# Kernel optimization log

Measured on AMD Instinct MI355X. Metric: run time of the kernel, lower is better.

Reference implementation:

```python
import jax, jax.numpy as jnp
import numpy as np

N_EMBD = 1024
HEAD_SIZE = 64

def setup_inputs() -> dict:
    key = jax.random.key(0)
    k1, k2, k3, k4 = jax.random.split(key, 4)
    x = jax.random.normal(k1, (8, 2048, N_EMBD), dtype=jnp.float32)
    s = 1.0 / np.sqrt(N_EMBD)
    Wk = jax.random.normal(k2, (HEAD_SIZE, N_EMBD), dtype=jnp.float32) * s
    Wq = jax.random.normal(k3, (HEAD_SIZE, N_EMBD), dtype=jnp.float32) * s
    Wv = jax.random.normal(k4, (HEAD_SIZE, N_EMBD), dtype=jnp.float32) * s
    return {"x": x, "Wk": Wk, "Wq": Wq, "Wv": Wv}

def reference(x, Wk, Wq, Wv):
    B, T, C = x.shape
    k = jnp.einsum('btc,hc->bth', x, Wk)  # [B,T,Hd]
    q = jnp.einsum('btc,hc->bth', x, Wq)
    v = jnp.einsum('btc,hc->bth', x, Wv)
    # NOTE: original scales by C**-0.5 where C = n_embd (not head_size)
    wei = jnp.einsum('bqh,bkh->bqk', q, k) * (C ** -0.5)  # [B,T,T]
    causal = jnp.tril(jnp.ones((T, T), dtype=bool))
    wei = jnp.where(causal, wei, -jnp.inf)
    wei = jax.nn.softmax(wei, axis=-1)
    out = jnp.einsum('bqk,bkh->bqh', wei, v)  # [B,T,Hd]
    return out
```

## Files before the change

kernel.cpp:

```cpp
#include <hip/hip_runtime.h>


typedef __attribute__((ext_vector_type(4))) short sv4;
typedef __attribute__((ext_vector_type(8))) short sv8;
typedef __attribute__((ext_vector_type(4))) float f32x4;

#define NB   8
#define TSEQ 2048
#define CDIM 1024
#define HD   64
#define MROWS (NB * TSEQ)

__device__ __forceinline__ short f2s(float f) {
  union { float f; unsigned u; } v; v.f = f;
  unsigned u = v.u;
  u += 0x7fffu + ((u >> 16) & 1u);
  return (short)(u >> 16);
}
__device__ __forceinline__ unsigned pk2(float lo, float hi) {
  return (unsigned)(unsigned short)f2s(lo) | ((unsigned)(unsigned short)f2s(hi) << 16);
}
__device__ __forceinline__ void glds16(const short* g, short* l) {
  __builtin_amdgcn_global_load_lds(
      (const __attribute__((address_space(1))) unsigned int*)g,
      (__attribute__((address_space(3))) unsigned int*)l, 16, 0, 0);
}

__global__ __launch_bounds__(256) void wcvt(
    const float* __restrict__ Wq, const float* __restrict__ Wk,
    const float* __restrict__ Wv, short* __restrict__ wb)
{
  int i = blockIdx.x * 256 + threadIdx.x;
  int t = i / 3072;
  int rem = i - t * 3072;
  int r = rem >> 4, s = rem & 15;
  int j = r >> 6, wrow = r & 63;
  const float* W = (j == 0) ? Wq : (j == 1) ? Wk : Wv;
  const float* src = W + (size_t)wrow * CDIM + t * 128 + ((s ^ (wrow & 7)) << 3);
  float4 a = *(const float4*)src;
  float4 b = *(const float4*)(src + 4);
  sv8 v = {f2s(a.x), f2s(a.y), f2s(a.z), f2s(a.w),
           f2s(b.x), f2s(b.y), f2s(b.z), f2s(b.w)};
  *(sv8*)(wb + (size_t)i * 8) = v;
}

__global__ __launch_bounds__(1024) void qkv_proj(
    const float* __restrict__ x,
    const short* __restrict__ wb,
    short* __restrict__ qw,
    short* __restrict__ kw,
    short* __restrict__ vtw)
{
  __shared__ short wlds[2][24576];
  __shared__ short xlds[2][8192];
  const int tid  = threadIdx.x;
  const int wid  = tid >> 6;
  const int lane = tid & 63;
  const int g    = lane >> 4;
  const int c16  = lane & 15;
  const int rowg = wid >> 2;
  const int ph   = wid & 3;
  const int row0 = blockIdx.x * 64;

  const int xr = tid >> 4, xs = tid & 15;
  const float* xsrc = x + (size_t)(row0 + xr) * CDIM + xs * 8;
  const int xwo = xr * 128 + ((xs ^ (xr & 7)) << 3);

  const int arow = rowg * 16 + c16;
  const int x7   = arow & 7;
  int rWo[3], rW7[3];
  #pragma unroll
  for (int p6 = 0; p6 < 3; ++p6) {
    int p = ph * 3 + p6;
    int r = (p >> 2) * 64 + (p & 3) * 16 + c16;
    rWo[p6] = r * 128;
    rW7[p6] = r & 7;
  }

  f32x4 acc[3];
  #pragma unroll
  for (int p6 = 0; p6 < 3; ++p6) acc[p6] = (f32x4){0.f, 0.f, 0.f, 0.f};

  float4 px[2][2];

  #pragma unroll
  for (int k2 = 0; k2 < 3; ++k2)
    glds16(wb + (size_t)(tid + k2 * 1024) * 8, &wlds[0][(tid + k2 * 1024) * 8]);
  px[0][0] = *(const float4*)(xsrc);
  px[0][1] = *(const float4*)(xsrc + 4);
  px[1][0] = *(const float4*)(xsrc + 128);
  px[1][1] = *(const float4*)(xsrc + 132);
  asm volatile("s_waitcnt vmcnt(2)" ::: "memory");
  {
    float4 A = px[0][0], B = px[0][1];
    sv8 v = {f2s(A.x), f2s(A.y), f2s(A.z), f2s(A.w),
             f2s(B.x), f2s(B.y), f2s(B.z), f2s(B.w)};
    *(sv8*)&xlds[0][xwo] = v;
  }
  asm volatile("s_waitcnt lgkmcnt(0)" ::: "memory");
  __builtin_amdgcn_sched_barrier(0);
  __builtin_amdgcn_s_barrier();

  #pragma unroll
  for (int t = 0; t < 8; ++t) {
    const int buf = t & 1;
    if (t < 7) {
      #pragma unroll
      for (int k2 = 0; k2 < 3; ++k2)
        glds16(wb + (size_t)((t + 1) * 3072 + tid + k2 * 1024) * 8,
               &wlds[buf ^ 1][(tid + k2 * 1024) * 8]);
    }
    if (t < 6) {
      px[t & 1][0] = *(const float4*)(xsrc + (t + 2) * 128);
      px[t & 1][1] = *(const float4*)(xsrc + (t + 2) * 128 + 4);
    }
    if (t < 7) {
      float4 A = px[(t + 1) & 1][0], B = px[(t + 1) & 1][1];
      sv8 v = {f2s(A.x), f2s(A.y), f2s(A.z), f2s(A.w),
               f2s(B.x), f2s(B.y), f2s(B.z), f2s(B.w)};
      *(sv8*)&xlds[buf ^ 1][xwo] = v;
    }
    #pragma unroll
    for (int kk = 0; kk < 4; ++kk) {
      int kslot = kk * 4 + g;
      sv8 a = *(const sv8*)&xlds[buf][arow * 128 + ((kslot ^ x7) << 3)];
      #pragma unroll
      for (int p6 = 0; p6 < 3; ++p6) {
        sv8 bfr = *(const sv8*)&wlds[buf][rWo[p6] + ((kslot ^ rW7[p6]) << 3)];
        acc[p6] = __builtin_amdgcn_mfma_f32_16x16x32_bf16(a, bfr, acc[p6], 0, 0, 0);
      }
    }
    if (t < 7) {
      if (t < 6) asm volatile("s_waitcnt vmcnt(2) lgkmcnt(0)" ::: "memory");
      else       asm volatile("s_waitcnt vmcnt(0) lgkmcnt(0)" ::: "memory");
      __builtin_amdgcn_sched_barrier(0);
      __builtin_amdgcn_s_barrier();
    }
  }

  #pragma unroll
  for (int p6 = 0; p6 < 3; ++p6) {
    int p = ph * 3 + p6, j = p >> 2, n = p & 3;
    int cc  = (n << 4) + c16;
    int rr0 = row0 + rowg * 16 + (g << 2);
    if (j == 2) {
      int b = rr0 >> 11, ti = rr0 & (TSEQ - 1);
      int kt = ti >> 6, key = ti & 63;
      sv4 v = {f2s(acc[p6][0]), f2s(acc[p6][1]), f2s(acc[p6][2]), f2s(acc[p6][3])};
      *(sv4*)&vtw[(((size_t)b * 32 + kt) * 64 + cc) * 64 +
                  ((((key >> 3) ^ (cc & 7)) << 3) | (key & 7))] = v;
    } else {
      #pragma unroll
      for (int r = 0; r < 4; ++r) {
        int rr = rr0 + r;
        if (j == 0) {
          qw[(size_t)rr * HD + cc] = f2s(acc[p6][r] * 0.03125f);
        } else {
          kw[(size_t)rr * HD + ((((cc >> 3) ^ (rr & 7)) << 3) | (cc & 7))] =
              f2s(acc[p6][r]);
        }
      }
    }
  }
}

__global__ __launch_bounds__(256) void attn(
    const short* __restrict__ qw,
    const short* __restrict__ kw,
    const short* __restrict__ vtw,
    float* __restrict__ Opart,
    float* __restrict__ mlws)
{
  __shared__ short kbuf[2][8192];
  __shared__ short vbuf[2][8192];
  __shared__ short bridge[4][2048];

  const int tid  = threadIdx.x;
  const int wid  = tid >> 6;
  const int lane = tid & 63;
  const int g    = lane >> 4;
  const int c16  = lane & 15;

  const int bid   = blockIdx.x;
  const int h     = bid >> 8;
  const int sub   = bid & 255;
  const int batch = sub & 7;
  const int jj    = sub >> 3;
  const int qb    = h ? (31 - jj) : jj;
  const int q0    = qb << 6;
  const size_t base = (size_t)batch * TSEQ * HD;

  const int ntot = (qb >> 1) + 1;
  const int th_  = (ntot + 1) >> 1;
  const int t0   = h ? th_ : 0;
  const int t1   = h ? ntot : th_;

  const int qrow = q0 + (wid << 4) + c16;
  sv8 qa0 = *(const sv8*)(qw + base + (size_t)qrow * HD + (g << 3));
  sv8 qa1 = *(const sv8*)(qw + base + (size_t)qrow * HD + 32 + (g << 3));

  float m = -1e30f, l = 0.f;
  f32x4 o[4];
  #pragma unroll
  for (int n = 0; n < 4; ++n) o[n] = (f32x4){0.f, 0.f, 0.f, 0.f};

  short* br = &bridge[wid][0];
  const int sx = c16 & 15;

  #define STAGE(tt, bb)                                                      \
    {                                                                        \
      const short* ksrc = kw + base + (size_t)(tt) * 8192;                   \
      const short* vsrc = vtw + ((size_t)batch * 32 + (tt) * 2) * 4096;      \
      _Pragma("unroll")                                                      \
      for (int q = 0; q < 4; ++q)                                            \
        glds16(ksrc + (tid + q * 256) * 8, &kbuf[bb][(tid + q * 256) * 8]);  \
      _Pragma("unroll")                                                      \
      for (int q = 0; q < 4; ++q)                                            \
        glds16(vsrc + (tid + q * 256) * 8, &vbuf[bb][(tid + q * 256) * 8]);  \
    }

  if (t0 < t1) {
    STAGE(t0, 0);
    asm volatile("s_waitcnt vmcnt(0)" ::: "memory");
    __builtin_amdgcn_s_barrier();

    for (int t = t0; t < t1; ++t) {
      const int buf = (t - t0) & 1;
      if (t + 1 < t1) STAGE(t + 1, buf ^ 1);

      f32x4 s[8];
      #pragma unroll
      for (int n = 0; n < 8; ++n) s[n] = (f32x4){0.f, 0.f, 0.f, 0.f};
      __builtin_amdgcn_s_setprio(1);
      #pragma unroll
      for (int n = 0; n < 8; ++n) {
        int kr = (n << 4) + c16;
        sv8 k0 = *(const sv8*)&kbuf[buf][kr * 64 + ((g ^ (kr & 7)) << 3)];
        s[n] = __builtin_amdgcn_mfma_f32_16x16x32_bf16(k0, qa0, s[n], 0, 0, 0);
        sv8 k1 = *(const sv8*)&kbuf[buf][kr * 64 + (((4 + g) ^ (kr & 7)) << 3)];
        s[n] = __builtin_amdgcn_mfma_f32_16x16x32_bf16(k1, qa1, s[n], 0, 0, 0);
      }
      __builtin_amdgcn_s_setprio(0);

      if (t == (qb >> 1)) {
        #pragma unroll
        for (int n = 0; n < 8; ++n) {
          int key = (t << 7) + (n << 4) + (g << 2);
          #pragma unroll
          for (int r = 0; r < 4; ++r)
            s[n][r] = (key + r <= qrow) ? s[n][r] : -1e30f;
        }
      }

      float pmax = -1e30f;
      #pragma unroll
      for (int n = 0; n < 8; ++n)
        pmax = fmaxf(pmax, fmaxf(fmaxf(s[n][0], s[n][1]), fmaxf(s[n][2], s[n][3])));
      float mnew  = m;
      float alpha = 1.f;
      const bool defer = (__all(pmax - m <= 8.0f) != 0);
      if (!defer) {
        float mx = fmaxf(pmax, __shfl_xor(pmax, 16));
        mx = fmaxf(mx, __shfl_xor(mx, 32));
        mnew  = fmaxf(m, mx);
        alpha = __expf(m - mnew);
        m = mnew;
      }

      float sum = 0.f;
      #pragma unroll
      for (int n = 0; n < 8; ++n) {
        float p0 = __expf(s[n][0] - mnew);
        float p1 = __expf(s[n][1] - mnew);
        float p2 = __expf(s[n][2] - mnew);
        float p3 = __expf(s[n][3] - mnew);
        sum += (p0 + p1) + (p2 + p3);
        int slot = 2 * n + (g >> 1);
        uint2 w2; w2.x = pk2(p0, p1); w2.y = pk2(p2, p3);
        *(uint2*)&br[c16 * 128 + ((slot ^ sx) << 3) + ((g & 1) << 2)] = w2;
      }
      sum += __shfl_xor(sum, 16);
      sum += __shfl_xor(sum, 32);

      if (!defer) {
        l = l * alpha + sum;
        float af[4];
        #pragma unroll
        for (int r = 0; r < 4; ++r) af[r] = __shfl(alpha, (g << 2) + r);
        #pragma unroll
        for (int n = 0; n < 4; ++n)
          #pragma unroll
          for (int r = 0; r < 4; ++r) o[n][r] *= af[r];
      } else {
        l += sum;
      }

      asm volatile("s_waitcnt lgkmcnt(0)" ::: "memory");
      __builtin_amdgcn_sched_barrier(0);

      __builtin_amdgcn_s_setprio(1);
      #pragma unroll
      for (int kk = 0; kk < 4; ++kk) {
        int kslot = (kk << 2) + g;
        sv8 pa = *(const sv8*)&br[c16 * 128 + ((kslot ^ sx) << 3)];
        #pragma unroll
        for (int n = 0; n < 4; ++n) {
          int vr = (n << 4) + c16;
          sv8 vf = *(const sv8*)&vbuf[buf][(kslot >> 3) * 4096 + vr * 64 +
                                           (((kslot & 7) ^ (vr & 7)) << 3)];
          o[n] = __builtin_amdgcn_mfma_f32_16x16x32_bf16(pa, vf, o[n], 0, 0, 0);
        }
      }
      __builtin_amdgcn_s_setprio(0);

      if (t + 1 < t1) {
        asm volatile("s_waitcnt vmcnt(0)" ::: "memory");
        __builtin_amdgcn_sched_barrier(0);
        __builtin_amdgcn_s_barrier();
      }
    }
  }

  #pragma unroll
  for (int n = 0; n < 4; ++n) {
    #pragma unroll
    for (int r = 0; r < 4; ++r) {
      int row = (wid << 4) + (g << 2) + r;
      Opart[(size_t)bid * 4096 + row * 64 + (n << 4) + c16] = o[n][r];
    }
  }
  if (lane < 16) {
    int row = (wid << 4) + lane;
    mlws[((size_t)bid * 64 + row) * 2]     = m;
    mlws[((size_t)bid * 64 + row) * 2 + 1] = l;
  }
  #undef STAGE
}

__global__ __launch_bounds__(256) void combine(
    const float* __restrict__ Opart,
    const float* __restrict__ mlws,
    float* __restrict__ out)
{
  const int bid   = blockIdx.x;
  const int batch = bid & 7;
  const int qb    = bid >> 3;
  const int q0    = qb << 6;
  const int bid0  = bid;
  const int bid1  = 256 + ((31 - qb) << 3) + batch;

  const int tid = threadIdx.x;
  const int row = tid >> 2;
  const int cs  = (tid & 3) << 4;

  float m0 = mlws[((size_t)bid0 * 64 + row) * 2];
  float l0 = mlws[((size_t)bid0 * 64 + row) * 2 + 1];
  float m1 = mlws[((size_t)bid1 * 64 + row) * 2];
  float l1 = mlws[((size_t)bid1 * 64 + row) * 2 + 1];
  float M  = fmaxf(m0, m1);
  float a0 = __expf(m0 - M), a1 = __expf(m1 - M);
  float invL = 1.f / (l0 * a0 + l1 * a1);

  const float* O0 = Opart + (size_t)bid0 * 4096 + row * 64 + cs;
  const float* O1 = Opart + (size_t)bid1 * 4096 + row * 64 + cs;
  float* op = out + ((size_t)batch * TSEQ + q0 + row) * HD + cs;

  #pragma unroll
  for (int e = 0; e < 4; ++e) {
    float4 v0 = *(const float4*)(O0 + e * 4);
    float4 v1 = *(const float4*)(O1 + e * 4);
    float4 res;
    res.x = (v0.x * a0 + v1.x * a1) * invL;
    res.y = (v0.y * a0 + v1.y * a1) * invL;
    res.z = (v0.z * a0 + v1.z * a1) * invL;
    res.w = (v0.w * a0 + v1.w * a1) * invL;
    *(float4*)(op + e * 4) = res;
  }
}

extern "C" void kernel_launch(void* const* d_in, const int* in_sizes, int n_in,
                              void* d_out, int out_size, void* d_ws, size_t ws_size,
                              hipStream_t stream) {
  const float* x  = (const float*)d_in[0];
  const float* Wk = (const float*)d_in[1];
  const float* Wq = (const float*)d_in[2];
  const float* Wv = (const float*)d_in[3];
  float* out = (float*)d_out;

  short* qw  = (short*)d_ws;
  short* kw  = qw + (size_t)MROWS * HD;
  short* vtw = kw + (size_t)MROWS * HD;
  short* wb  = vtw + (size_t)NB * HD * TSEQ;
  float* Opart = (float*)(wb + 24576 * 8);
  float* mlws  = Opart + (size_t)512 * 4096;

  wcvt<<<dim3(96), dim3(256), 0, stream>>>(Wq, Wk, Wv, wb);
  qkv_proj<<<dim3(MROWS / 64), dim3(1024), 0, stream>>>(x, wb, qw, kw, vtw);
  attn<<<dim3(512), dim3(256), 0, stream>>>(qw, kw, vtw, Opart, mlws);
  combine<<<dim3(256), dim3(256), 0, stream>>>(Opart, mlws, out);
}
```

Baseline: 51.26 us.

## Merge split-KV halves into one 512-thread block and fuse combine via LDS

```diff
diff --git a/kernel.cpp b/kernel.cpp
--- a/kernel.cpp
+++ b/kernel.cpp
@@ -164,38 +164,37 @@
   }
 }
 
-__global__ __launch_bounds__(256) void attn(
+__global__ __launch_bounds__(512) void attn(
     const short* __restrict__ qw,
     const short* __restrict__ kw,
     const short* __restrict__ vtw,
-    float* __restrict__ Opart,
-    float* __restrict__ mlws)
+    float* __restrict__ out)
 {
-  __shared__ short kbuf[2][8192];
-  __shared__ short vbuf[2][8192];
-  __shared__ short bridge[4][2048];
+  __shared__ short kbuf[2][2][8192];
+  __shared__ short vbuf[2][2][8192];
+  __shared__ short bridge[8][1024];
 
   const int tid  = threadIdx.x;
   const int wid  = tid >> 6;
+  const int h    = wid >> 2;
+  const int lwid = wid & 3;
+  const int ltid = tid & 255;
   const int lane = tid & 63;
   const int g    = lane >> 4;
   const int c16  = lane & 15;
 
   const int bid   = blockIdx.x;
-  const int h     = bid >> 8;
-  const int sub   = bid & 255;
-  const int batch = sub & 7;
-  const int jj    = sub >> 3;
-  const int qb    = h ? (31 - jj) : jj;
+  const int batch = bid & 7;
+  const int qb    = bid >> 3;
   const int q0    = qb << 6;
   const size_t base = (size_t)batch * TSEQ * HD;
 
   const int ntot = (qb >> 1) + 1;
   const int th_  = (ntot + 1) >> 1;
   const int t0   = h ? th_ : 0;
-  const int t1   = h ? ntot : th_;
-
-  const int qrow = q0 + (wid << 4) + c16;
+  const int cnt  = h ? (ntot - th_) : th_;
+
+  const int qrow = q0 + (lwid << 4) + c16;
   sv8 qa0 = *(const sv8*)(qw + base + (size_t)qrow * HD + (g << 3));
   sv8 qa1 = *(const sv8*)(qw + base + (size_t)qrow * HD + 32 + (g << 3));
 
@@ -205,29 +204,31 @@
   for (int n = 0; n < 4; ++n) o[n] = (f32x4){0.f, 0.f, 0.f, 0.f};
 
   short* br = &bridge[wid][0];
-  const int sx = c16 & 15;
-
-  #define STAGE(tt, bb)                                                      \
-    {                                                                        \
-      const short* ksrc = kw + base + (size_t)(tt) * 8192;                   \
-      const short* vsrc = vtw + ((size_t)batch * 32 + (tt) * 2) * 4096;      \
-      _Pragma("unroll")                                                      \
-      for (int q = 0; q < 4; ++q)                                            \
-        glds16(ksrc + (tid + q * 256) * 8, &kbuf[bb][(tid + q * 256) * 8]);  \
-      _Pragma("unroll")                                                      \
-      for (int q = 0; q < 4; ++q)                                            \
-        glds16(vsrc + (tid + q * 256) * 8, &vbuf[bb][(tid + q * 256) * 8]);  \
-    }
-
-  if (t0 < t1) {
-    STAGE(t0, 0);
-    asm volatile("s_waitcnt vmcnt(0)" ::: "memory");
-    __builtin_amdgcn_s_barrier();
-
-    for (int t = t0; t < t1; ++t) {
-      const int buf = (t - t0) & 1;
-      if (t + 1 < t1) STAGE(t + 1, buf ^ 1);
-
+  const int sx7 = c16 & 7;
+
+  #define STAGE(tt, bb)                                                        \
+    {                                                                          \
+      const short* ksrc = kw + base + (size_t)(tt) * 8192;                     \
+      const short* vsrc = vtw + ((size_t)batch * 32 + (tt) * 2) * 4096;        \
+      _Pragma("unroll")                                                        \
+      for (int q = 0; q < 4; ++q)                                              \
+        glds16(ksrc + (ltid + q * 256) * 8, &kbuf[h][bb][(ltid + q * 256) * 8]);\
+      _Pragma("unroll")                                                        \
+      for (int q = 0; q < 4; ++q)                                              \
+        glds16(vsrc + (ltid + q * 256) * 8, &vbuf[h][bb][(ltid + q * 256) * 8]);\
+    }
+
+  if (cnt > 0) STAGE(t0, 0);
+  asm volatile("s_waitcnt vmcnt(0)" ::: "memory");
+  __builtin_amdgcn_s_barrier();
+
+  for (int it = 0; it < th_; ++it) {
+    const int t   = t0 + it;
+    const int buf = it & 1;
+    const bool valid = it < cnt;
+    if (valid && (it + 1 < cnt)) STAGE(t + 1, buf ^ 1);
+
+    if (valid) {
       f32x4 s[8];
       #pragma unroll
       for (int n = 0; n < 8; ++n) s[n] = (f32x4){0.f, 0.f, 0.f, 0.f};
@@ -235,9 +236,9 @@
       #pragma unroll
       for (int n = 0; n < 8; ++n) {
         int kr = (n << 4) + c16;
-        sv8 k0 = *(const sv8*)&kbuf[buf][kr * 64 + ((g ^ (kr & 7)) << 3)];
+        sv8 k0 = *(const sv8*)&kbuf[h][buf][kr * 64 + ((g ^ (kr & 7)) << 3)];
         s[n] = __builtin_amdgcn_mfma_f32_16x16x32_bf16(k0, qa0, s[n], 0, 0, 0);
-        sv8 k1 = *(const sv8*)&kbuf[buf][kr * 64 + (((4 + g) ^ (kr & 7)) << 3)];
+        sv8 k1 = *(const sv8*)&kbuf[h][buf][kr * 64 + (((4 + g) ^ (kr & 7)) << 3)];
         s[n] = __builtin_amdgcn_mfma_f32_16x16x32_bf16(k1, qa1, s[n], 0, 0, 0);
       }
       __builtin_amdgcn_s_setprio(0);
@@ -257,32 +258,29 @@
       for (int n = 0; n < 8; ++n)
         pmax = fmaxf(pmax, fmaxf(fmaxf(s[n][0], s[n][1]), fmaxf(s[n][2], s[n][3])));
       float mnew  = m;
-      float alpha = 1.f;
       const bool defer = (__all(pmax - m <= 8.0f) != 0);
       if (!defer) {
         float mx = fmaxf(pmax, __shfl_xor(pmax, 16));
         mx = fmaxf(mx, __shfl_xor(mx, 32));
-        mnew  = fmaxf(m, mx);
-        alpha = __expf(m - mnew);
-        m = mnew;
+        mnew = fmaxf(m, mx);
       }
 
       float sum = 0.f;
       #pragma unroll
       for (int n = 0; n < 8; ++n) {
-        float p0 = __expf(s[n][0] - mnew);
-        float p1 = __expf(s[n][1] - mnew);
-        float p2 = __expf(s[n][2] - mnew);
-        float p3 = __expf(s[n][3] - mnew);
-        sum += (p0 + p1) + (p2 + p3);
-        int slot = 2 * n + (g >> 1);
-        uint2 w2; w2.x = pk2(p0, p1); w2.y = pk2(p2, p3);
-        *(uint2*)&br[c16 * 128 + ((slot ^ sx) << 3) + ((g & 1) << 2)] = w2;
+        #pragma unroll
+        for (int r = 0; r < 4; ++r) {
+          float p = __expf(s[n][r] - mnew);
+          s[n][r] = p;
+          sum += p;
+        }
       }
       sum += __shfl_xor(sum, 16);
       sum += __shfl_xor(sum, 32);
 
       if (!defer) {
+        float alpha = __expf(m - mnew);
+        m = mnew;
         l = l * alpha + sum;
         float af[4];
         #pragma unroll
@@ -295,87 +293,78 @@
         l += sum;
       }
 
-      asm volatile("s_waitcnt lgkmcnt(0)" ::: "memory");
-      __builtin_amdgcn_sched_barrier(0);
-
-      __builtin_amdgcn_s_setprio(1);
-      #pragma unroll
-      for (int kk = 0; kk < 4; ++kk) {
-        int kslot = (kk << 2) + g;
-        sv8 pa = *(const sv8*)&br[c16 * 128 + ((kslot ^ sx) << 3)];
+      #pragma unroll
+      for (int hv = 0; hv < 2; ++hv) {
         #pragma unroll
         for (int n = 0; n < 4; ++n) {
-          int vr = (n << 4) + c16;
-          sv8 vf = *(const sv8*)&vbuf[buf][(kslot >> 3) * 4096 + vr * 64 +
-                                           (((kslot & 7) ^ (vr & 7)) << 3)];
-          o[n] = __builtin_amdgcn_mfma_f32_16x16x32_bf16(pa, vf, o[n], 0, 0, 0);
-        }
-      }
-      __builtin_amdgcn_s_setprio(0);
-
-      if (t + 1 < t1) {
-        asm volatile("s_waitcnt vmcnt(0)" ::: "memory");
+          int nn = (hv << 2) + n;
+          int slot = 2 * n + (g >> 1);
+          uint2 w2;
+          w2.x = pk2(s[nn][0], s[nn][1]);
+          w2.y = pk2(s[nn][2], s[nn][3]);
+          *(uint2*)&br[(c16 << 6) + ((slot ^ sx7) << 3) + ((g & 1) << 2)] = w2;
+        }
+        asm volatile("s_waitcnt lgkmcnt(0)" ::: "memory");
         __builtin_amdgcn_sched_barrier(0);
-        __builtin_amdgcn_s_barrier();
-      }
-    }
-  }
-
-  #pragma unroll
-  for (int n = 0; n < 4; ++n) {
+        __builtin_amdgcn_s_setprio(1);
+        #pragma unroll
+        for (int kk = 0; kk < 2; ++kk) {
+          int kslot = (((hv << 1) + kk) << 2) + g;
+          sv8 pa = *(const sv8*)&br[(c16 << 6) + ((((kk << 2) + g) ^ sx7) << 3)];
+          #pragma unroll
+          for (int n = 0; n < 4; ++n) {
+            int vr = (n << 4) + c16;
+            sv8 vf = *(const sv8*)&vbuf[h][buf][(kslot >> 3) * 4096 + vr * 64 +
+                                               (((kslot & 7) ^ (vr & 7)) << 3)];
+            o[n] = __builtin_amdgcn_mfma_f32_16x16x32_bf16(pa, vf, o[n], 0, 0, 0);
+          }
+        }
+        __builtin_amdgcn_s_setprio(0);
+      }
+    }
+
+    asm volatile("s_waitcnt vmcnt(0)" ::: "memory");
+    __builtin_amdgcn_sched_barrier(0);
+    __builtin_amdgcn_s_barrier();
+  }
+
+  float* OLDS = (float*)&kbuf[0][0][0];
+  float* mlds = OLDS + 4096;
+  float* llds = mlds + 64;
+
+  if (h == 1) {
+    #pragma unroll
+    for (int n = 0; n < 4; ++n) {
+      #pragma unroll
+      for (int r = 0; r < 4; ++r) {
+        int row = (lwid << 4) + (g << 2) + r;
+        OLDS[row * 64 + (n << 4) + c16] = o[n][r];
+      }
+    }
+    if (lane < 16) {
+      mlds[(lwid << 4) + lane] = m;
+      llds[(lwid << 4) + lane] = l;
+    }
+  }
+  __syncthreads();
+  if (h == 0) {
     #pragma unroll
     for (int r = 0; r < 4; ++r) {
-      int row = (wid << 4) + (g << 2) + r;
-      Opart[(size_t)bid * 4096 + row * 64 + (n << 4) + c16] = o[n][r];
-    }
-  }
-  if (lane < 16) {
-    int row = (wid << 4) + lane;
-    mlws[((size_t)bid * 64 + row) * 2]     = m;
-    mlws[((size_t)bid * 64 + row) * 2 + 1] = l;
+      int row = (lwid << 4) + (g << 2) + r;
+      float m0 = __shfl(m, (g << 2) + r);
+      float l0 = __shfl(l, (g << 2) + r);
+      float m1 = mlds[row], l1 = llds[row];
+      float M  = fmaxf(m0, m1);
+      float a0 = __expf(m0 - M), a1 = __expf(m1 - M);
+      float invL = 1.f / (l0 * a0 + l1 * a1);
+      #pragma unroll
+      for (int n = 0; n < 4; ++n) {
+        float v = (o[n][r] * a0 + OLDS[row * 64 + (n << 4) + c16] * a1) * invL;
+        out[base + (size_t)(q0 + row) * HD + (n << 4) + c16] = v;
+      }
+    }
   }
   #undef STAGE
-}
-
-__global__ __launch_bounds__(256) void combine(
-    const float* __restrict__ Opart,
-    const float* __restrict__ mlws,
-    float* __restrict__ out)
-{
-  const int bid   = blockIdx.x;
-  const int batch = bid & 7;
-  const int qb    = bid >> 3;
-  const int q0    = qb << 6;
-  const int bid0  = bid;
-  const int bid1  = 256 + ((31 - qb) << 3) + batch;
-
-  const int tid = threadIdx.x;
-  const int row = tid >> 2;
-  const int cs  = (tid & 3) << 4;
-
-  float m0 = mlws[((size_t)bid0 * 64 + row) * 2];
-  float l0 = mlws[((size_t)bid0 * 64 + row) * 2 + 1];
-  float m1 = mlws[((size_t)bid1 * 64 + row) * 2];
-  float l1 = mlws[((size_t)bid1 * 64 + row) * 2 + 1];
-  float M  = fmaxf(m0, m1);
-  float a0 = __expf(m0 - M), a1 = __expf(m1 - M);
-  float invL = 1.f / (l0 * a0 + l1 * a1);
-
-  const float* O0 = Opart + (size_t)bid0 * 4096 + row * 64 + cs;
-  const float* O1 = Opart + (size_t)bid1 * 4096 + row * 64 + cs;
-  float* op = out + ((size_t)batch * TSEQ + q0 + row) * HD + cs;
-
-  #pragma unroll
-  for (int e = 0; e < 4; ++e) {
-    float4 v0 = *(const float4*)(O0 + e * 4);
-    float4 v1 = *(const float4*)(O1 + e * 4);
-    float4 res;
-    res.x = (v0.x * a0 + v1.x * a1) * invL;
-    res.y = (v0.y * a0 + v1.y * a1) * invL;
-    res.z = (v0.z * a0 + v1.z * a1) * invL;
-    res.w = (v0.w * a0 + v1.w * a1) * invL;
-    *(float4*)(op + e * 4) = res;
-  }
 }
 
 extern "C" void kernel_launch(void* const* d_in, const int* in_sizes, int n_in,
@@ -391,11 +380,8 @@
   short* kw  = qw + (size_t)MROWS * HD;
   short* vtw = kw + (size_t)MROWS * HD;
   short* wb  = vtw + (size_t)NB * HD * TSEQ;
-  float* Opart = (float*)(wb + 24576 * 8);
-  float* mlws  = Opart + (size_t)512 * 4096;
 
   wcvt<<<dim3(96), dim3(256), 0, stream>>>(Wq, Wk, Wv, wb);
   qkv_proj<<<dim3(MROWS / 64), dim3(1024), 0, stream>>>(x, wb, qw, kw, vtw);
-  attn<<<dim3(512), dim3(256), 0, stream>>>(qw, kw, vtw, Opart, mlws);
-  combine<<<dim3(256), dim3(256), 0, stream>>>(Opart, mlws, out);
-}
+  attn<<<dim3(256), dim3(512), 0, stream>>>(qw, kw, vtw, out);
+}
```

After: 49.19 us, median of 2. 4.0% less time.

## Fuse split-KV combine into attention kernel via last-arriver atomic counter

Applied to the files above, without the earlier changes.

```diff
diff --git a/kernel.cpp b/kernel.cpp
--- a/kernel.cpp
+++ b/kernel.cpp
@@ -28,8 +28,10 @@
 
 __global__ __launch_bounds__(256) void wcvt(
     const float* __restrict__ Wq, const float* __restrict__ Wk,
-    const float* __restrict__ Wv, short* __restrict__ wb)
+    const float* __restrict__ Wv, short* __restrict__ wb,
+    unsigned* __restrict__ cnt)
 {
+  if (blockIdx.x == 0) cnt[threadIdx.x] = 0;
   int i = blockIdx.x * 256 + threadIdx.x;
   int t = i / 3072;
   int rem = i - t * 3072;
@@ -169,11 +171,14 @@
     const short* __restrict__ kw,
     const short* __restrict__ vtw,
     float* __restrict__ Opart,
-    float* __restrict__ mlws)
+    float* __restrict__ mlws,
+    unsigned* __restrict__ cnt,
+    float* __restrict__ out)
 {
   __shared__ short kbuf[2][8192];
   __shared__ short vbuf[2][8192];
   __shared__ short bridge[4][2048];
+  __shared__ unsigned ordsh;
 
   const int tid  = threadIdx.x;
   const int wid  = tid >> 6;
@@ -183,10 +188,11 @@
 
   const int bid   = blockIdx.x;
   const int h     = bid >> 8;
-  const int sub   = bid & 255;
-  const int batch = sub & 7;
-  const int jj    = sub >> 3;
+  const int sub_  = bid & 255;
+  const int batch = sub_ & 7;
+  const int jj    = sub_ >> 3;
   const int qb    = h ? (31 - jj) : jj;
+  const int sub   = (qb << 3) | batch;
   const int q0    = qb << 6;
   const size_t base = (size_t)batch * TSEQ * HD;
 
@@ -297,7 +303,6 @@
 
       asm volatile("s_waitcnt lgkmcnt(0)" ::: "memory");
       __builtin_amdgcn_sched_barrier(0);
-
       __builtin_amdgcn_s_setprio(1);
       #pragma unroll
       for (int kk = 0; kk < 4; ++kk) {
@@ -321,61 +326,53 @@
     }
   }
 
+  float* myO = Opart + (size_t)(sub * 2 + h) * 4096;
   #pragma unroll
   for (int n = 0; n < 4; ++n) {
     #pragma unroll
     for (int r = 0; r < 4; ++r) {
       int row = (wid << 4) + (g << 2) + r;
-      Opart[(size_t)bid * 4096 + row * 64 + (n << 4) + c16] = o[n][r];
+      myO[row * 64 + (n << 4) + c16] = o[n][r];
     }
   }
   if (lane < 16) {
     int row = (wid << 4) + lane;
-    mlws[((size_t)bid * 64 + row) * 2]     = m;
-    mlws[((size_t)bid * 64 + row) * 2 + 1] = l;
+    mlws[((size_t)(sub * 2 + h) * 64 + row) * 2]     = m;
+    mlws[((size_t)(sub * 2 + h) * 64 + row) * 2 + 1] = l;
+  }
+
+  __threadfence();
+  __syncthreads();
+  if (tid == 0) ordsh = atomicAdd(&cnt[sub], 1u);
+  __syncthreads();
+  if (ordsh == 1u) {
+    __threadfence();
+    const int oh = h ^ 1;
+    const float* oO  = Opart + (size_t)(sub * 2 + oh) * 4096;
+    const float* oml = mlws + (size_t)(sub * 2 + oh) * 128;
+    #pragma unroll
+    for (int r = 0; r < 4; ++r) {
+      int row = (wid << 4) + (g << 2) + r;
+      float mm = __shfl(m, (g << 2) + r);
+      float ll = __shfl(l, (g << 2) + r);
+      float mo = oml[row * 2], lo = oml[row * 2 + 1];
+      float m0 = (h == 0) ? mm : mo;
+      float l0 = (h == 0) ? ll : lo;
+      float m1 = (h == 0) ? mo : mm;
+      float l1 = (h == 0) ? lo : ll;
+      float M  = fmaxf(m0, m1);
+      float a0 = __expf(m0 - M), a1 = __expf(m1 - M);
+      float invL = 1.f / (l0 * a0 + l1 * a1);
+      float amine = (h == 0) ? a0 : a1;
+      float aoth  = (h == 0) ? a1 : a0;
+      #pragma unroll
+      for (int n = 0; n < 4; ++n) {
+        float v = (o[n][r] * amine + oO[row * 64 + (n << 4) + c16] * aoth) * invL;
+        out[base + (size_t)(q0 + row) * HD + (n << 4) + c16] = v;
+      }
+    }
   }
   #undef STAGE
-}
-
-__global__ __launch_bounds__(256) void combine(
-    const float* __restrict__ Opart,
-    const float* __restrict__ mlws,
-    float* __restrict__ out)
-{
-  const int bid   = blockIdx.x;
-  const int batch = bid & 7;
-  const int qb    = bid >> 3;
-  const int q0    = qb << 6;
-  const int bid0  = bid;
-  const int bid1  = 256 + ((31 - qb) << 3) + batch;
-
-  const int tid = threadIdx.x;
-  const int row = tid >> 2;
-  const int cs  = (tid & 3) << 4;
-
-  float m0 = mlws[((size_t)bid0 * 64 + row) * 2];
-  float l0 = mlws[((size_t)bid0 * 64 + row) * 2 + 1];
-  float m1 = mlws[((size_t)bid1 * 64 + row) * 2];
-  float l1 = mlws[((size_t)bid1 * 64 + row) * 2 + 1];
-  float M  = fmaxf(m0, m1);
-  float a0 = __expf(m0 - M), a1 = __expf(m1 - M);
-  float invL = 1.f / (l0 * a0 + l1 * a1);
-
-  const float* O0 = Opart + (size_t)bid0 * 4096 + row * 64 + cs;
-  const float* O1 = Opart + (size_t)bid1 * 4096 + row * 64 + cs;
-  float* op = out + ((size_t)batch * TSEQ + q0 + row) * HD + cs;
-
-  #pragma unroll
-  for (int e = 0; e < 4; ++e) {
-    float4 v0 = *(const float4*)(O0 + e * 4);
-    float4 v1 = *(const float4*)(O1 + e * 4);
-    float4 res;
-    res.x = (v0.x * a0 + v1.x * a1) * invL;
-    res.y = (v0.y * a0 + v1.y * a1) * invL;
-    res.z = (v0.z * a0 + v1.z * a1) * invL;
-    res.w = (v0.w * a0 + v1.w * a1) * invL;
-    *(float4*)(op + e * 4) = res;
-  }
 }
 
 extern "C" void kernel_launch(void* const* d_in, const int* in_sizes, int n_in,
@@ -391,11 +388,11 @@
   short* kw  = qw + (size_t)MROWS * HD;
   short* vtw = kw + (size_t)MROWS * HD;
   short* wb  = vtw + (size_t)NB * HD * TSEQ;
-  float* Opart = (float*)(wb + 24576 * 8);
+  float* Opart = (float*)(wb + (size_t)24576 * 8);
   float* mlws  = Opart + (size_t)512 * 4096;
-
-  wcvt<<<dim3(96), dim3(256), 0, stream>>>(Wq, Wk, Wv, wb);
+  unsigned* cnt = (unsigned*)(mlws + (size_t)512 * 128);
+
+  wcvt<<<dim3(96), dim3(256), 0, stream>>>(Wq, Wk, Wv, wb, cnt);
   qkv_proj<<<dim3(MROWS / 64), dim3(1024), 0, stream>>>(x, wb, qw, kw, vtw);
-  attn<<<dim3(512), dim3(256), 0, stream>>>(qw, kw, vtw, Opart, mlws);
-  combine<<<dim3(256), dim3(256), 0, stream>>>(Opart, mlws, out);
-}
+  attn<<<dim3(512), dim3(256), 0, stream>>>(qw, kw, vtw, Opart, mlws, cnt, out);
+}
```

Measured after the change: 121.3 us. 2.37x slower.
